# Optimization experiments

Hardware: AMD Instinct MI355X
Metric: run time of the kernel (lower is better)

## Reference

```python
import jax, jax.numpy as jnp
import numpy as np

MODEL_D = 512
N_HEADS = 8
D_K = 64
D_V = 64
EPS = 1e-5


def _layer_norm(x, g, b):
    mu = jnp.mean(x, axis=-1, keepdims=True)
    var = jnp.mean((x - mu) ** 2, axis=-1, keepdims=True)
    return (x - mu) * jax.lax.rsqrt(var + EPS) * g + b


def setup_inputs() -> dict:
    key = jax.random.key(0)
    ks = jax.random.split(key, 8)
    B, S = 8, 1024
    smiles = jax.random.normal(ks[0], (B, S, MODEL_D), dtype=jnp.float32)
    # causal mask: True where attention is disallowed (masked_fill semantics)
    mask = jnp.broadcast_to(jnp.triu(jnp.ones((S, S), dtype=bool), k=1), (B, S, S))
    sd = 1.0 / np.sqrt(MODEL_D)
    w_q = jax.random.normal(ks[1], (MODEL_D, N_HEADS * D_K), dtype=jnp.float32) * sd
    w_k = jax.random.normal(ks[2], (MODEL_D, N_HEADS * D_K), dtype=jnp.float32) * sd
    w_v = jax.random.normal(ks[3], (MODEL_D, N_HEADS * D_V), dtype=jnp.float32) * sd
    w_o = jax.random.normal(ks[4], (N_HEADS * D_V, MODEL_D), dtype=jnp.float32) * sd
    w1 = jax.random.normal(ks[5], (MODEL_D, 4 * MODEL_D), dtype=jnp.float32) * sd
    w2 = jax.random.normal(ks[6], (4 * MODEL_D, MODEL_D), dtype=jnp.float32) * (1.0 / np.sqrt(4 * MODEL_D))
    ln1_g = jnp.ones((MODEL_D,), jnp.float32)
    ln1_b = jnp.zeros((MODEL_D,), jnp.float32)
    ln2_g = jnp.ones((MODEL_D,), jnp.float32)
    ln2_b = jnp.zeros((MODEL_D,), jnp.float32)
    return {"smiles": smiles, "mask": mask, "w_q": w_q, "w_k": w_k, "w_v": w_v,
            "w_o": w_o, "ln1_g": ln1_g, "ln1_b": ln1_b, "w1": w1, "w2": w2,
            "ln2_g": ln2_g, "ln2_b": ln2_b}


def reference(smiles, mask, w_q, w_k, w_v, w_o, ln1_g, ln1_b, w1, w2, ln2_g, ln2_b):
    B, S, _ = smiles.shape
    # QKV projections -> [B, H, S, d]
    q = (smiles @ w_q).reshape(B, S, N_HEADS, D_K).transpose(0, 2, 1, 3)
    k = (smiles @ w_k).reshape(B, S, N_HEADS, D_K).transpose(0, 2, 1, 3)
    v = (smiles @ w_v).reshape(B, S, N_HEADS, D_V).transpose(0, 2, 1, 3)
    scores = jnp.einsum("bhqd,bhkd->bhqk", q, k) / np.sqrt(D_K)
    scores = jnp.where(mask[:, None, :, :], jnp.float32(-1e9), scores)
    attention = jax.nn.softmax(scores, axis=-1)
    ctx = jnp.einsum("bhqk,bhkd->bhqd", attention, v)
    ctx = ctx.transpose(0, 2, 1, 3).reshape(B, S, N_HEADS * D_V)
    attn_out = _layer_norm(ctx @ w_o + smiles, ln1_g, ln1_b)
    ffn = jax.nn.relu(attn_out @ w1) @ w2
    out = _layer_norm(ffn + attn_out, ln2_g, ln2_b)
    return out, attention
```

## Files before the change

kernel.cpp:

```cpp
#include <hip/hip_runtime.h>
#include <math.h>

#define BATCH 8
#define SEQ   1024
#define DMODEL 512
#define NHEADS 8
#define DKV   64
#define DFF   2048
#define ROWS  (BATCH * SEQ)
#define QKLD  1536

typedef __attribute__((ext_vector_type(8))) short short8;
typedef __attribute__((ext_vector_type(4))) float f32x4;

__device__ __forceinline__ short f2bf(float f) {
    unsigned u = __float_as_uint(f);
    u += 0x7FFFu + ((u >> 16) & 1u);
    return (short)(u >> 16);
}
__device__ __forceinline__ float bf2f(short s) {
    return __uint_as_float(((unsigned)(unsigned short)s) << 16);
}

#define GLD16(g, l) __builtin_amdgcn_global_load_lds( \
    (const __attribute__((address_space(1))) void*)(g), \
    (__attribute__((address_space(3))) void*)(l), 16, 0, 0)

__device__ __forceinline__ void stage128x32(const short* __restrict__ g, int ld,
                                            short* lds, int tid) {
    const int w = tid >> 6;
#pragma unroll
    for (int i = 0; i < 2; ++i) {
        const int L = i * 256 + tid;
        const int r = L >> 2, c = (L & 3) << 3;
        GLD16(g + (size_t)r * ld + c, lds + (size_t)(i * 256 + (w << 6)) * 8);
    }
}

template<int OUT_BF16, int RELU>
__global__ __launch_bounds__(256) void gemm_bt(const short* __restrict__ A,
                                               const short* __restrict__ Bt,
                                               void* __restrict__ Cv,
                                               int K, int lda, int ldb, int ldc,
                                               int qcols) {
    __shared__ short As[2][128 * 32];
    __shared__ short Bs[2][128 * 32];
    const int tid = threadIdx.x;
    const int m0 = blockIdx.y * 128, n0 = blockIdx.x * 128;
    const int w = tid >> 6, lane = tid & 63;
    const int wr = (w >> 1) * 64, wc = (w & 1) * 64;
    const int lrow = lane & 15, hi = lane >> 4;

    f32x4 acc[4][4];
#pragma unroll
    for (int m = 0; m < 4; ++m)
#pragma unroll
        for (int n = 0; n < 4; ++n) acc[m][n] = {0.f, 0.f, 0.f, 0.f};

    const short* Ab = A + (size_t)m0 * lda;
    const short* Bb = Bt + (size_t)n0 * ldb;
    const int nt = K >> 5;

    stage128x32(Ab, lda, As[0], tid);
    stage128x32(Bb, ldb, Bs[0], tid);
    __syncthreads();

    int cur = 0;
    for (int t = 0; t < nt; ++t) {
        if (t + 1 < nt) {
            stage128x32(Ab + (size_t)(t + 1) * 32, lda, As[cur ^ 1], tid);
            stage128x32(Bb + (size_t)(t + 1) * 32, ldb, Bs[cur ^ 1], tid);
        }

        short8 af[4], bfr[4];
#pragma unroll
        for (int m = 0; m < 4; ++m)
            af[m] = *(const short8*)&As[cur][(size_t)(wr + m * 16 + lrow) * 32 + hi * 8];
#pragma unroll
        for (int n = 0; n < 4; ++n)
            bfr[n] = *(const short8*)&Bs[cur][(size_t)(wc + n * 16 + lrow) * 32 + hi * 8];
#pragma unroll
        for (int m = 0; m < 4; ++m)
#pragma unroll
            for (int n = 0; n < 4; ++n)
                acc[m][n] = __builtin_amdgcn_mfma_f32_16x16x32_bf16(bfr[n], af[m], acc[m][n], 0, 0, 0);

        __syncthreads();
        cur ^= 1;
    }

    const int orow = m0 + wr + lrow;
    const int ocol0 = n0 + wc + hi * 4;
#pragma unroll
    for (int m = 0; m < 4; ++m)
#pragma unroll
        for (int n = 0; n < 4; ++n) {
            const int col = ocol0 + n * 16;
            const float cs = (col < qcols) ? 0.125f : 1.0f;
            float v0 = acc[m][n][0], v1 = acc[m][n][1], v2 = acc[m][n][2], v3 = acc[m][n][3];
            if (RELU) {
                v0 = fmaxf(v0, 0.f); v1 = fmaxf(v1, 0.f);
                v2 = fmaxf(v2, 0.f); v3 = fmaxf(v3, 0.f);
            }
            v0 *= cs; v1 *= cs; v2 *= cs; v3 *= cs;
            const size_t off = (size_t)(orow + m * 16) * ldc + col;
            if (OUT_BF16) {
                short4 st = { f2bf(v0), f2bf(v1), f2bf(v2), f2bf(v3) };
                *(short4*)((short*)Cv + off) = st;
            } else {
                float4 st = { v0, v1, v2, v3 };
                *(float4*)((float*)Cv + off) = st;
            }
        }
}

__global__ __launch_bounds__(256, 2) void fused_attn(const short* __restrict__ Q,
                                                     const short* __restrict__ K,
                                                     const short* __restrict__ Vt,
                                                     float* __restrict__ attnP,
                                                     short* __restrict__ ctx) {
    const int it = 7 - blockIdx.x, bh = blockIdx.y, b = bh >> 3, h = bh & 7;
    __shared__ short Qs[128 * 64];
    __shared__ short Ks[128 * 64];
    __shared__ short Vs[64 * 128];
    __shared__ short Ps[128 * 128];
    float* rsum = (float*)Ps;

    const int tid = threadIdx.x;
    const int w = tid >> 6, lane = tid & 63;
    const int wr = (w >> 1) * 64, wc2 = (w & 1);
    const int lrow = lane & 15, hi = lane >> 4;
    const size_t base = (size_t)b * SEQ * QKLD + h * DKV;
    float* aprow = attnP + (size_t)bh * SEQ * SEQ;

    {
        const int nz4 = (7 - it) * 32;
        if (nz4 > 0) {
            for (int r = tid >> 5; r < 128; r += 8) {
                float4* rp = (float4*)(aprow + (size_t)(it * 128 + r) * SEQ + (it + 1) * 128);
                for (int c = tid & 31; c < nz4; c += 32)
                    rp[c] = make_float4(0.f, 0.f, 0.f, 0.f);
            }
        }
    }

#pragma unroll
    for (int i = 0; i < 4; ++i) {
        const int L = i * 256 + tid;
        const int r = L >> 3, sc = ((L & 7) ^ (r & 7)) * 8;
        GLD16(Q + base + (size_t)(it * 128 + r) * QKLD + sc,
              Qs + (size_t)(i * 256 + (w << 6)) * 8);
    }

    float rs[4] = {0.f, 0.f, 0.f, 0.f};

    for (int kt = 0; kt <= it; ++kt) {
#pragma unroll
        for (int i = 0; i < 4; ++i) {
            const int L = i * 256 + tid;
            const int r = L >> 3, sc = ((L & 7) ^ (r & 7)) * 8;
            GLD16(K + base + (size_t)(kt * 128 + r) * QKLD + sc,
                  Ks + (size_t)(i * 256 + (w << 6)) * 8);
        }
        __syncthreads();

        f32x4 s[4][4];
#pragma unroll
        for (int m = 0; m < 4; ++m)
#pragma unroll
            for (int n = 0; n < 4; ++n) s[m][n] = {0.f, 0.f, 0.f, 0.f};
#pragma unroll
        for (int sk = 0; sk < 2; ++sk) {
            short8 qf[4], kf[4];
#pragma unroll
            for (int m = 0; m < 4; ++m) {
                const int r = wr + m * 16 + lrow;
                qf[m] = *(const short8*)((const char*)Qs + r * 128 + ((hi * 16 + sk * 64) ^ ((r & 7) << 4)));
            }
#pragma unroll
            for (int n = 0; n < 4; ++n) {
                const int r = wc2 * 64 + n * 16 + lrow;
                kf[n] = *(const short8*)((const char*)Ks + r * 128 + ((hi * 16 + sk * 64) ^ ((r & 7) << 4)));
            }
#pragma unroll
            for (int m = 0; m < 4; ++m)
#pragma unroll
                for (int n = 0; n < 4; ++n)
                    s[m][n] = __builtin_amdgcn_mfma_f32_16x16x32_bf16(kf[n], qf[m], s[m][n], 0, 0, 0);
        }

        const bool diag = (kt == it);
#pragma unroll
        for (int m = 0; m < 4; ++m) {
            const int q = wr + m * 16 + lrow;
#pragma unroll
            for (int n = 0; n < 4; ++n) {
                const int k0 = wc2 * 64 + n * 16 + hi * 4;
#pragma unroll
                for (int r = 0; r < 4; ++r) {
                    float p = __expf(s[m][n][r]);
                    if (diag && k0 + r > q) p = 0.f;
                    rs[m] += p;
                }
            }
        }
        __syncthreads();
    }

#pragma unroll
    for (int m = 0; m < 4; ++m) {
        rs[m] += __shfl_xor(rs[m], 16);
        rs[m] += __shfl_xor(rs[m], 32);
    }
    if (lane < 16) {
#pragma unroll
        for (int m = 0; m < 4; ++m)
            rsum[wc2 * 128 + wr + m * 16 + lane] = rs[m];
    }
    __syncthreads();
    if (tid < 128) rsum[tid] = 1.0f / (rsum[tid] + rsum[128 + tid]);
    __syncthreads();
    float inv[4];
#pragma unroll
    for (int m = 0; m < 4; ++m) inv[m] = rsum[wr + m * 16 + lrow];
    __syncthreads();

    f32x4 o[4][2];
#pragma unroll
    for (int m = 0; m < 4; ++m)
#pragma unroll
        for (int n = 0; n < 2; ++n) o[m][n] = {0.f, 0.f, 0.f, 0.f};

    for (int kt = 0; kt <= it; ++kt) {
#pragma unroll
        for (int i = 0; i < 4; ++i) {
            const int L = i * 256 + tid;
            const int r = L >> 3, sc = ((L & 7) ^ (r & 7)) * 8;
            GLD16(K + base + (size_t)(kt * 128 + r) * QKLD + sc,
                  Ks + (size_t)(i * 256 + (w << 6)) * 8);
        }
#pragma unroll
        for (int i = 0; i < 4; ++i) {
            const int L = i * 256 + tid;
            const int r = L >> 4, sc = ((L & 15) ^ (r & 7)) * 8;
            GLD16(Vt + (size_t)(bh * DKV + r) * SEQ + kt * 128 + sc,
                  Vs + (size_t)(i * 256 + (w << 6)) * 8);
        }
        __syncthreads();

        f32x4 s[4][4];
#pragma unroll
        for (int m = 0; m < 4; ++m)
#pragma unroll
            for (int n = 0; n < 4; ++n) s[m][n] = {0.f, 0.f, 0.f, 0.f};
#pragma unroll
        for (int sk = 0; sk < 2; ++sk) {
            short8 qf[4], kf[4];
#pragma unroll
            for (int m = 0; m < 4; ++m) {
                const int r = wr + m * 16 + lrow;
                qf[m] = *(const short8*)((const char*)Qs + r * 128 + ((hi * 16 + sk * 64) ^ ((r & 7) << 4)));
            }
#pragma unroll
            for (int n = 0; n < 4; ++n) {
                const int r = wc2 * 64 + n * 16 + lrow;
                kf[n] = *(const short8*)((const char*)Ks + r * 128 + ((hi * 16 + sk * 64) ^ ((r & 7) << 4)));
            }
#pragma unroll
            for (int m = 0; m < 4; ++m)
#pragma unroll
                for (int n = 0; n < 4; ++n)
                    s[m][n] = __builtin_amdgcn_mfma_f32_16x16x32_bf16(kf[n], qf[m], s[m][n], 0, 0, 0);
        }

        const bool diag = (kt == it);
#pragma unroll
        for (int m = 0; m < 4; ++m) {
            const int q = wr + m * 16 + lrow;
#pragma unroll
            for (int n = 0; n < 4; ++n) {
                const int k0 = wc2 * 64 + n * 16 + hi * 4;
                float p0 = __expf(s[m][n][0]);
                float p1 = __expf(s[m][n][1]);
                float p2 = __expf(s[m][n][2]);
                float p3 = __expf(s[m][n][3]);
                if (diag) {
                    if (k0 + 0 > q) p0 = 0.f;
                    if (k0 + 1 > q) p1 = 0.f;
                    if (k0 + 2 > q) p2 = 0.f;
                    if (k0 + 3 > q) p3 = 0.f;
                }
                p0 *= inv[m]; p1 *= inv[m]; p2 *= inv[m]; p3 *= inv[m];
                float4 pv4 = { p0, p1, p2, p3 };
                *(float4*)(aprow + (size_t)(it * 128 + q) * SEQ + kt * 128 + k0) = pv4;
                short4 ph = { f2bf(p0), f2bf(p1), f2bf(p2), f2bf(p3) };
                *(short4*)((char*)Ps + q * 256 + ((k0 * 2) ^ ((q & 7) << 4))) = ph;
            }
        }
        __syncthreads();

#pragma unroll
        for (int sk = 0; sk < 4; ++sk) {
            short8 pf[4], vf[2];
#pragma unroll
            for (int m = 0; m < 4; ++m) {
                const int r = wr + m * 16 + lrow;
                pf[m] = *(const short8*)((const char*)Ps + r * 256 + ((hi * 16 + sk * 64) ^ ((r & 7) << 4)));
            }
#pragma unroll
            for (int n = 0; n < 2; ++n) {
                const int r = wc2 * 32 + n * 16 + lrow;
                vf[n] = *(const short8*)((const char*)Vs + r * 256 + ((hi * 16 + sk * 64) ^ ((r & 7) << 4)));
            }
#pragma unroll
            for (int m = 0; m < 4; ++m)
#pragma unroll
                for (int n = 0; n < 2; ++n)
                    o[m][n] = __builtin_amdgcn_mfma_f32_16x16x32_bf16(vf[n], pf[m], o[m][n], 0, 0, 0);
        }
        __syncthreads();
    }

#pragma unroll
    for (int m = 0; m < 4; ++m) {
        const int q = it * 128 + wr + m * 16 + lrow;
#pragma unroll
        for (int n = 0; n < 2; ++n) {
            const int d = h * DKV + wc2 * 32 + n * 16 + hi * 4;
            short4 st = { f2bf(o[m][n][0]), f2bf(o[m][n][1]),
                          f2bf(o[m][n][2]), f2bf(o[m][n][3]) };
            *(short4*)(ctx + (size_t)(b * SEQ + q) * DMODEL + d) = st;
        }
    }
}

template<int RES_BF16, int OUT_F32, int OUT_BF16>
__global__ __launch_bounds__(128) void residual_ln(const float* __restrict__ xin,
                                                   const void* __restrict__ res,
                                                   const float* __restrict__ g,
                                                   const float* __restrict__ beta,
                                                   float* __restrict__ outf,
                                                   short* __restrict__ outh) {
    const int row = blockIdx.x;
    const int tid = threadIdx.x;

    float4 v = ((const float4*)(xin + (size_t)row * DMODEL))[tid];
    if (RES_BF16) {
        const short4 rr = ((const short4*)((const short*)res + (size_t)row * DMODEL))[tid];
        v.x += bf2f(rr.x); v.y += bf2f(rr.y); v.z += bf2f(rr.z); v.w += bf2f(rr.w);
    } else {
        const float4 rr = ((const float4*)((const float*)res + (size_t)row * DMODEL))[tid];
        v.x += rr.x; v.y += rr.y; v.z += rr.z; v.w += rr.w;
    }

    float sum = v.x + v.y + v.z + v.w;
    float sq  = v.x * v.x + v.y * v.y + v.z * v.z + v.w * v.w;
#pragma unroll
    for (int off = 32; off > 0; off >>= 1) {
        sum += __shfl_down(sum, off);
        sq  += __shfl_down(sq, off);
    }
    __shared__ float s_sum[2], s_sq[2];
    const int wid = tid >> 6, lane = tid & 63;
    if (lane == 0) { s_sum[wid] = sum; s_sq[wid] = sq; }
    __syncthreads();

    const float tsum = s_sum[0] + s_sum[1];
    const float tsq  = s_sq[0] + s_sq[1];
    const float mu   = tsum * (1.0f / DMODEL);
    const float var  = tsq * (1.0f / DMODEL) - mu * mu;
    const float rstd = rsqrtf(var + 1e-5f);

    const float4 gg = ((const float4*)g)[tid];
    const float4 bb = ((const float4*)beta)[tid];
    float4 o;
    o.x = (v.x - mu) * rstd * gg.x + bb.x;
    o.y = (v.y - mu) * rstd * gg.y + bb.y;
    o.z = (v.z - mu) * rstd * gg.z + bb.z;
    o.w = (v.w - mu) * rstd * gg.w + bb.w;
    if (OUT_F32) ((float4*)(outf + (size_t)row * DMODEL))[tid] = o;
    if (OUT_BF16) {
        short4 oh = { f2bf(o.x), f2bf(o.y), f2bf(o.z), f2bf(o.w) };
        ((short4*)(outh + (size_t)row * DMODEL))[tid] = oh;
    }
}

__global__ __launch_bounds__(256) void convert_bf16(const float* __restrict__ X,
                                                    short* __restrict__ Xh) {
    const size_t i = (size_t)blockIdx.x * 256 + threadIdx.x;
    const float4* p = (const float4*)X + i * 2;
    const float4 a = p[0], b = p[1];
    short8 o = { f2bf(a.x), f2bf(a.y), f2bf(a.z), f2bf(a.w),
                 f2bf(b.x), f2bf(b.y), f2bf(b.z), f2bf(b.w) };
    *(short8*)(Xh + i * 8) = o;
}

__global__ __launch_bounds__(256) void transpose_w(const float* __restrict__ W,
                                                   short* __restrict__ Wt,
                                                   int K, int N) {
    __shared__ float t[32][33];
    const int n0 = blockIdx.x * 32, k0 = blockIdx.y * 32;
    const int tx = threadIdx.x, ty = threadIdx.y;
#pragma unroll
    for (int i = 0; i < 4; ++i)
        t[ty + i * 8][tx] = W[(size_t)(k0 + ty + i * 8) * N + n0 + tx];
    __syncthreads();
#pragma unroll
    for (int i = 0; i < 4; ++i)
        Wt[(size_t)(n0 + ty + i * 8) * K + k0 + tx] = f2bf(t[tx][ty + i * 8]);
}

__global__ __launch_bounds__(256) void transpose_v(const short* __restrict__ QKV,
                                                   short* __restrict__ Vt) {
    __shared__ short t[32][33];
    const int s0 = blockIdx.x * 32, d0 = blockIdx.y * 32, bh = blockIdx.z;
    const int b = bh >> 3, h = bh & 7;
    const int tx = threadIdx.x, ty = threadIdx.y;
#pragma unroll
    for (int i = 0; i < 4; ++i)
        t[ty + i * 8][tx] = QKV[(size_t)(b * SEQ + s0 + ty + i * 8) * QKLD + 1024 + h * DKV + d0 + tx];
    __syncthreads();
#pragma unroll
    for (int i = 0; i < 4; ++i)
        Vt[(size_t)(bh * DKV + d0 + ty + i * 8) * SEQ + s0 + tx] = t[tx][ty + i * 8];
}

extern "C" void kernel_launch(void* const* d_in, const int* in_sizes, int n_in,
                              void* d_out, int out_size, void* d_ws, size_t ws_size,
                              hipStream_t stream) {
    const float* X    = (const float*)d_in[0];
    const float* w_q  = (const float*)d_in[2];
    const float* w_k  = (const float*)d_in[3];
    const float* w_v  = (const float*)d_in[4];
    const float* w_o  = (const float*)d_in[5];
    const float* ln1g = (const float*)d_in[6];
    const float* ln1b = (const float*)d_in[7];
    const float* w1   = (const float*)d_in[8];
    const float* w2   = (const float*)d_in[9];
    const float* ln2g = (const float*)d_in[10];
    const float* ln2b = (const float*)d_in[11];

    float* out   = (float*)d_out;
    float* attnP = out + (size_t)ROWS * DMODEL;

    const size_t M = 1u << 20;
    short* ws    = (short*)d_ws;
    short* qkv   = ws;
    short* Vt    = ws + 12 * M;
    short* ctxh  = ws + 16 * M;
    short* aoutH = ws + 20 * M;
    short* Xh    = ws + 24 * M;
    short* wqkvt = ws + 28 * M;
    short* wot   = wqkvt + 786432;
    short* w1t   = ws + 29 * M;
    short* w2t   = ws + 30 * M;
    short* hbuf  = ws;

    convert_bf16<<<dim3(2048), dim3(256), 0, stream>>>(X, Xh);
    transpose_w<<<dim3(16, 16), dim3(32, 8), 0, stream>>>(w_q, wqkvt, DMODEL, DMODEL);
    transpose_w<<<dim3(16, 16), dim3(32, 8), 0, stream>>>(w_k, wqkvt + 512 * 512, DMODEL, DMODEL);
    transpose_w<<<dim3(16, 16), dim3(32, 8), 0, stream>>>(w_v, wqkvt + 1024 * 512, DMODEL, DMODEL);
    transpose_w<<<dim3(16, 16), dim3(32, 8), 0, stream>>>(w_o, wot, DMODEL, DMODEL);
    transpose_w<<<dim3(64, 16), dim3(32, 8), 0, stream>>>(w1, w1t, DMODEL, DFF);
    transpose_w<<<dim3(16, 64), dim3(32, 8), 0, stream>>>(w2, w2t, DFF, DMODEL);

    gemm_bt<1, 0><<<dim3(12, 64), dim3(256), 0, stream>>>(Xh, wqkvt, qkv,
                                                          DMODEL, DMODEL, DMODEL, QKLD, 512);
    transpose_v<<<dim3(32, 2, 64), dim3(32, 8), 0, stream>>>(qkv, Vt);

    fused_attn<<<dim3(8, 64), dim3(256), 0, stream>>>(qkv, qkv + 512, Vt, attnP, ctxh);

    gemm_bt<0, 0><<<dim3(4, 64), dim3(256), 0, stream>>>(ctxh, wot, out,
                                                         DMODEL, DMODEL, DMODEL, DMODEL, 0);
    residual_ln<0, 0, 1><<<dim3(ROWS), dim3(128), 0, stream>>>(out, X, ln1g, ln1b, nullptr, aoutH);

    gemm_bt<1, 1><<<dim3(16, 64), dim3(256), 0, stream>>>(aoutH, w1t, hbuf,
                                                          DMODEL, DMODEL, DMODEL, DFF, 0);
    gemm_bt<0, 0><<<dim3(4, 64), dim3(256), 0, stream>>>(hbuf, w2t, out,
                                                         DFF, DFF, DFF, DMODEL, 0);
    residual_ln<1, 1, 0><<<dim3(ROWS), dim3(128), 0, stream>>>(out, aoutH, ln2g, ln2b, out, nullptr);
}
```

Measured before the change: 252.4 us.

## Restructure fused attention into PV-first pass with deferred normalization and prefetching

The attention kernel now does the P·V accumulation in its first pass using unnormalized exponentials, accumulating row sums alongside, and scales the context by the inverse sum at the end. A second pass recomputes QK^T only to write the normalized probability matrix, using double-buffered K tiles prefetched one step ahead. K/V loads in the first pass are issued right after their buffers are consumed, to overlap with compute. Both the GEMM and the attention grids also get a flat-index swizzle that changes which tiles run concurrently, for cache locality. This removes the dedicated sum-only pass's V-free redundant work but keeps two QK passes; P is rounded to bf16 before normalization, which slightly changes numerics.

```diff
diff --git a/kernel.cpp b/kernel.cpp
--- a/kernel.cpp
+++ b/kernel.cpp
@@ -46,7 +46,13 @@
     __shared__ short As[2][128 * 32];
     __shared__ short Bs[2][128 * 32];
     const int tid = threadIdx.x;
-    const int m0 = blockIdx.y * 128, n0 = blockIdx.x * 128;
+
+    const int nx = gridDim.x;
+    const int nwg = nx * gridDim.y;
+    const int flat = blockIdx.y * nx + blockIdx.x;
+    const int swz = (flat & 7) * (nwg >> 3) + (flat >> 3);
+    const int m0 = (swz / nx) * 128, n0 = (swz % nx) * 128;
+
     const int w = tid >> 6, lane = tid & 63;
     const int wr = (w >> 1) * 64, wc = (w & 1) * 64;
     const int lrow = lane & 15, hi = lane >> 4;
@@ -119,10 +125,13 @@
                                                      const short* __restrict__ Vt,
                                                      float* __restrict__ attnP,
                                                      short* __restrict__ ctx) {
-    const int it = 7 - blockIdx.x, bh = blockIdx.y, b = bh >> 3, h = bh & 7;
+    const int flat = blockIdx.y * 8 + blockIdx.x;
+    const int swz  = (flat & 7) * 64 + (flat >> 3);
+    const int bh = swz >> 3, it = 7 - (swz & 7);
+    const int b = bh >> 3, h = bh & 7;
+
     __shared__ short Qs[128 * 64];
-    __shared__ short Ks[128 * 64];
-    __shared__ short Vs[64 * 128];
+    __shared__ short KVs[2][128 * 64];
     __shared__ short Ps[128 * 128];
     float* rsum = (float*)Ps;
 
@@ -132,6 +141,50 @@
     const int lrow = lane & 15, hi = lane >> 4;
     const size_t base = (size_t)b * SEQ * QKLD + h * DKV;
     float* aprow = attnP + (size_t)bh * SEQ * SEQ;
+
+    auto stage_k = [&](int kt, short* dst) {
+#pragma unroll
+        for (int i = 0; i < 4; ++i) {
+            const int L = i * 256 + tid;
+            const int r = L >> 3, sc = ((L & 7) ^ (r & 7)) * 8;
+            GLD16(K + base + (size_t)(kt * 128 + r) * QKLD + sc,
+                  dst + (size_t)(i * 256 + (w << 6)) * 8);
+        }
+    };
+    auto stage_v = [&](int kt, short* dst) {
+#pragma unroll
+        for (int i = 0; i < 4; ++i) {
+            const int L = i * 256 + tid;
+            const int r = L >> 4, sc = ((L & 15) ^ (r & 7)) * 8;
+            GLD16(Vt + (size_t)(bh * DKV + r) * SEQ + kt * 128 + sc,
+                  dst + (size_t)(i * 256 + (w << 6)) * 8);
+        }
+    };
+    auto qkt = [&](const short* Ks, f32x4 s[4][4]) {
+#pragma unroll
+        for (int m = 0; m < 4; ++m)
+#pragma unroll
+            for (int n = 0; n < 4; ++n) s[m][n] = {0.f, 0.f, 0.f, 0.f};
+#pragma unroll
+        for (int sk = 0; sk < 2; ++sk) {
+            short8 qf[4], kf[4];
+#pragma unroll
+            for (int m = 0; m < 4; ++m) {
+                const int r = wr + m * 16 + lrow;
+                qf[m] = *(const short8*)((const char*)Qs + r * 128 + ((hi * 16 + sk * 64) ^ ((r & 7) << 4)));
+            }
+#pragma unroll
+            for (int n = 0; n < 4; ++n) {
+                const int r = wc2 * 64 + n * 16 + lrow;
+                kf[n] = *(const short8*)((const char*)Ks + r * 128 + ((hi * 16 + sk * 64) ^ ((r & 7) << 4)));
+            }
+#pragma unroll
+            for (int m = 0; m < 4; ++m)
+#pragma unroll
+                for (int n = 0; n < 4; ++n)
+                    s[m][n] = __builtin_amdgcn_mfma_f32_16x16x32_bf16(kf[n], qf[m], s[m][n], 0, 0, 0);
+        }
+    };
 
     {
         const int nz4 = (7 - it) * 32;
@@ -151,127 +204,20 @@
         GLD16(Q + base + (size_t)(it * 128 + r) * QKLD + sc,
               Qs + (size_t)(i * 256 + (w << 6)) * 8);
     }
+    stage_k(0, KVs[0]);
+    stage_v(0, KVs[1]);
+    __syncthreads();
 
     float rs[4] = {0.f, 0.f, 0.f, 0.f};
+    f32x4 o[4][2];
+#pragma unroll
+    for (int m = 0; m < 4; ++m)
+#pragma unroll
+        for (int n = 0; n < 2; ++n) o[m][n] = {0.f, 0.f, 0.f, 0.f};
 
     for (int kt = 0; kt <= it; ++kt) {
-#pragma unroll
-        for (int i = 0; i < 4; ++i) {
-            const int L = i * 256 + tid;
-            const int r = L >> 3, sc = ((L & 7) ^ (r & 7)) * 8;
-            GLD16(K + base + (size_t)(kt * 128 + r) * QKLD + sc,
-                  Ks + (size_t)(i * 256 + (w << 6)) * 8);
-        }
-        __syncthreads();
-
         f32x4 s[4][4];
-#pragma unroll
-        for (int m = 0; m < 4; ++m)
-#pragma unroll
-            for (int n = 0; n < 4; ++n) s[m][n] = {0.f, 0.f, 0.f, 0.f};
-#pragma unroll
-        for (int sk = 0; sk < 2; ++sk) {
-            short8 qf[4], kf[4];
-#pragma unroll
-            for (int m = 0; m < 4; ++m) {
-                const int r = wr + m * 16 + lrow;
-                qf[m] = *(const short8*)((const char*)Qs + r * 128 + ((hi * 16 + sk * 64) ^ ((r & 7) << 4)));
-            }
-#pragma unroll
-            for (int n = 0; n < 4; ++n) {
-                const int r = wc2 * 64 + n * 16 + lrow;
-                kf[n] = *(const short8*)((const char*)Ks + r * 128 + ((hi * 16 + sk * 64) ^ ((r & 7) << 4)));
-            }
-#pragma unroll
-            for (int m = 0; m < 4; ++m)
-#pragma unroll
-                for (int n = 0; n < 4; ++n)
-                    s[m][n] = __builtin_amdgcn_mfma_f32_16x16x32_bf16(kf[n], qf[m], s[m][n], 0, 0, 0);
-        }
-
-        const bool diag = (kt == it);
-#pragma unroll
-        for (int m = 0; m < 4; ++m) {
-            const int q = wr + m * 16 + lrow;
-#pragma unroll
-            for (int n = 0; n < 4; ++n) {
-                const int k0 = wc2 * 64 + n * 16 + hi * 4;
-#pragma unroll
-                for (int r = 0; r < 4; ++r) {
-                    float p = __expf(s[m][n][r]);
-                    if (diag && k0 + r > q) p = 0.f;
-                    rs[m] += p;
-                }
-            }
-        }
-        __syncthreads();
-    }
-
-#pragma unroll
-    for (int m = 0; m < 4; ++m) {
-        rs[m] += __shfl_xor(rs[m], 16);
-        rs[m] += __shfl_xor(rs[m], 32);
-    }
-    if (lane < 16) {
-#pragma unroll
-        for (int m = 0; m < 4; ++m)
-            rsum[wc2 * 128 + wr + m * 16 + lane] = rs[m];
-    }
-    __syncthreads();
-    if (tid < 128) rsum[tid] = 1.0f / (rsum[tid] + rsum[128 + tid]);
-    __syncthreads();
-    float inv[4];
-#pragma unroll
-    for (int m = 0; m < 4; ++m) inv[m] = rsum[wr + m * 16 + lrow];
-    __syncthreads();
-
-    f32x4 o[4][2];
-#pragma unroll
-    for (int m = 0; m < 4; ++m)
-#pragma unroll
-        for (int n = 0; n < 2; ++n) o[m][n] = {0.f, 0.f, 0.f, 0.f};
-
-    for (int kt = 0; kt <= it; ++kt) {
-#pragma unroll
-        for (int i = 0; i < 4; ++i) {
-            const int L = i * 256 + tid;
-            const int r = L >> 3, sc = ((L & 7) ^ (r & 7)) * 8;
-            GLD16(K + base + (size_t)(kt * 128 + r) * QKLD + sc,
-                  Ks + (size_t)(i * 256 + (w << 6)) * 8);
-        }
-#pragma unroll
-        for (int i = 0; i < 4; ++i) {
-            const int L = i * 256 + tid;
-            const int r = L >> 4, sc = ((L & 15) ^ (r & 7)) * 8;
-            GLD16(Vt + (size_t)(bh * DKV + r) * SEQ + kt * 128 + sc,
-                  Vs + (size_t)(i * 256 + (w << 6)) * 8);
-        }
-        __syncthreads();
-
-        f32x4 s[4][4];
-#pragma unroll
-        for (int m = 0; m < 4; ++m)
-#pragma unroll
-            for (int n = 0; n < 4; ++n) s[m][n] = {0.f, 0.f, 0.f, 0.f};
-#pragma unroll
-        for (int sk = 0; sk < 2; ++sk) {
-            short8 qf[4], kf[4];
-#pragma unroll
-            for (int m = 0; m < 4; ++m) {
-                const int r = wr + m * 16 + lrow;
-                qf[m] = *(const short8*)((const char*)Qs + r * 128 + ((hi * 16 + sk * 64) ^ ((r & 7) << 4)));
-            }
-#pragma unroll
-            for (int n = 0; n < 4; ++n) {
-                const int r = wc2 * 64 + n * 16 + lrow;
-                kf[n] = *(const short8*)((const char*)Ks + r * 128 + ((hi * 16 + sk * 64) ^ ((r & 7) << 4)));
-            }
-#pragma unroll
-            for (int m = 0; m < 4; ++m)
-#pragma unroll
-                for (int n = 0; n < 4; ++n)
-                    s[m][n] = __builtin_amdgcn_mfma_f32_16x16x32_bf16(kf[n], qf[m], s[m][n], 0, 0, 0);
-        }
+        qkt(KVs[0], s);
 
         const bool diag = (kt == it);
 #pragma unroll
@@ -290,14 +236,13 @@
                     if (k0 + 2 > q) p2 = 0.f;
                     if (k0 + 3 > q) p3 = 0.f;
                 }
-                p0 *= inv[m]; p1 *= inv[m]; p2 *= inv[m]; p3 *= inv[m];
-                float4 pv4 = { p0, p1, p2, p3 };
-                *(float4*)(aprow + (size_t)(it * 128 + q) * SEQ + kt * 128 + k0) = pv4;
+                rs[m] += (p0 + p1) + (p2 + p3);
                 short4 ph = { f2bf(p0), f2bf(p1), f2bf(p2), f2bf(p3) };
                 *(short4*)((char*)Ps + q * 256 + ((k0 * 2) ^ ((q & 7) << 4))) = ph;
             }
         }
         __syncthreads();
+        if (kt < it) stage_k(kt + 1, KVs[0]);
 
 #pragma unroll
         for (int sk = 0; sk < 4; ++sk) {
@@ -310,7 +255,7 @@
 #pragma unroll
             for (int n = 0; n < 2; ++n) {
                 const int r = wc2 * 32 + n * 16 + lrow;
-                vf[n] = *(const short8*)((const char*)Vs + r * 256 + ((hi * 16 + sk * 64) ^ ((r & 7) << 4)));
+                vf[n] = *(const short8*)((const char*)KVs[1] + r * 256 + ((hi * 16 + sk * 64) ^ ((r & 7) << 4)));
             }
 #pragma unroll
             for (int m = 0; m < 4; ++m)
@@ -319,7 +264,25 @@
                     o[m][n] = __builtin_amdgcn_mfma_f32_16x16x32_bf16(vf[n], pf[m], o[m][n], 0, 0, 0);
         }
         __syncthreads();
-    }
+        if (kt < it) stage_v(kt + 1, KVs[1]);
+    }
+
+#pragma unroll
+    for (int m = 0; m < 4; ++m) {
+        rs[m] += __shfl_xor(rs[m], 16);
+        rs[m] += __shfl_xor(rs[m], 32);
+    }
+    if (lane < 16) {
+#pragma unroll
+        for (int m = 0; m < 4; ++m)
+            rsum[wc2 * 128 + wr + m * 16 + lane] = rs[m];
+    }
+    __syncthreads();
+    if (tid < 128) rsum[tid] = 1.0f / (rsum[tid] + rsum[128 + tid]);
+    __syncthreads();
+    float inv[4];
+#pragma unroll
+    for (int m = 0; m < 4; ++m) inv[m] = rsum[wr + m * 16 + lrow];
 
 #pragma unroll
     for (int m = 0; m < 4; ++m) {
@@ -327,10 +290,44 @@
 #pragma unroll
         for (int n = 0; n < 2; ++n) {
             const int d = h * DKV + wc2 * 32 + n * 16 + hi * 4;
-            short4 st = { f2bf(o[m][n][0]), f2bf(o[m][n][1]),
-                          f2bf(o[m][n][2]), f2bf(o[m][n][3]) };
+            short4 st = { f2bf(o[m][n][0] * inv[m]), f2bf(o[m][n][1] * inv[m]),
+                          f2bf(o[m][n][2] * inv[m]), f2bf(o[m][n][3] * inv[m]) };
             *(short4*)(ctx + (size_t)(b * SEQ + q) * DMODEL + d) = st;
         }
+    }
+
+    stage_k(0, KVs[0]);
+    __syncthreads();
+    int cur = 0;
+    for (int kt = 0; kt <= it; ++kt) {
+        if (kt < it) stage_k(kt + 1, KVs[cur ^ 1]);
+
+        f32x4 s[4][4];
+        qkt(KVs[cur], s);
+
+        const bool diag = (kt == it);
+#pragma unroll
+        for (int m = 0; m < 4; ++m) {
+            const int q = wr + m * 16 + lrow;
+#pragma unroll
+            for (int n = 0; n < 4; ++n) {
+                const int k0 = wc2 * 64 + n * 16 + hi * 4;
+                float p0 = __expf(s[m][n][0]);
+                float p1 = __expf(s[m][n][1]);
+                float p2 = __expf(s[m][n][2]);
+                float p3 = __expf(s[m][n][3]);
+                if (diag) {
+                    if (k0 + 0 > q) p0 = 0.f;
+                    if (k0 + 1 > q) p1 = 0.f;
+                    if (k0 + 2 > q) p2 = 0.f;
+                    if (k0 + 3 > q) p3 = 0.f;
+                }
+                float4 pv4 = { p0 * inv[m], p1 * inv[m], p2 * inv[m], p3 * inv[m] };
+                *(float4*)(aprow + (size_t)(it * 128 + q) * SEQ + kt * 128 + k0) = pv4;
+            }
+        }
+        __syncthreads();
+        cur ^= 1;
     }
 }
 
```

Result: faster. 234.9 us (-6.9%).
